# Performance work log

Hardware: AMD Instinct MI355X
Metric: run time of the kernel (lower is better)

## Reference

```python
import math
import jax, jax.numpy as jnp
import numpy as np

N_HEAD = 8
EPS = 1e-4

def _ln(x, g, b):
    m = jnp.mean(x, axis=-1, keepdims=True)
    v = jnp.mean((x - m) ** 2, axis=-1, keepdims=True)
    return (x - m) * jax.lax.rsqrt(v + EPS) * g + b

def _rel_bias(T, rel_w):
    # rel_pos_mat[i,j] = j - i, shifted to [0, 2T-2]; one-hot @ W == table lookup
    pos = jnp.arange(T)
    idx = pos[None, :] - pos[:, None] + (T - 1)        # [T,T]
    return rel_w[idx].transpose(2, 0, 1)               # [n_head,T,T]

def _attn(x, qw, qb, kw, kb, vw, vb, pw, pb, rel_pos):
    B, T, C = x.shape
    hd = C // N_HEAD
    q = (x @ qw + qb).reshape(B, T, N_HEAD, hd)
    k = (x @ kw + kb).reshape(B, T, N_HEAD, hd)
    v = (x @ vw + vb).reshape(B, T, N_HEAD, hd)
    att = jnp.einsum('bqhd,bkhd->bhqk', q, k) * (1.0 / math.sqrt(hd))
    att = att + rel_pos[None]
    att = jax.nn.softmax(att, axis=-1)
    y = jnp.einsum('bhqk,bkhd->bqhd', att, v).reshape(B, T, C)
    return y @ pw + pb

def setup_inputs() -> dict:
    key = jax.random.key(0)
    C, H, W, B = 512, 64, 64, 8
    ks = iter(jax.random.split(key, 40))
    d = {}
    d['x'] = jax.random.normal(next(ks), (B, H * W, C), jnp.float32)
    def w(shape):
        return jax.random.normal(next(ks), shape, jnp.float32) * 0.02
    for p in ('row', 'col'):
        for nm in ('q', 'k', 'v', 'p'):
            d[f'{p}_{nm}w'] = w((C, C))
            d[f'{p}_{nm}b'] = jnp.zeros((C,), jnp.float32)
    for nm in ('rln1', 'cln1', 'ln2'):
        d[f'{nm}_g'] = jnp.ones((C,), jnp.float32)
        d[f'{nm}_b'] = jnp.zeros((C,), jnp.float32)
    d['ff_w1'] = w((C, 4 * C)); d['ff_b1'] = jnp.zeros((4 * C,), jnp.float32)
    d['ff_w2'] = w((4 * C, C)); d['ff_b2'] = jnp.zeros((C,), jnp.float32)
    d['row_rel_w'] = w((2 * H - 1, N_HEAD))
    d['col_rel_w'] = w((2 * W - 1, N_HEAD))
    return d

def reference(x,
              row_qw, row_qb, row_kw, row_kb, row_vw, row_vb, row_pw, row_pb,
              col_qw, col_qb, col_kw, col_kb, col_vw, col_vb, col_pw, col_pb,
              rln1_g, rln1_b, cln1_g, cln1_b, ln2_g, ln2_b,
              ff_w1, ff_b1, ff_w2, ff_b2, row_rel_w, col_rel_w):
    b, n, c = x.shape
    h = w = int(math.isqrt(n))
    # row attention: over h within each column -> batch b*w
    xr = x.reshape(b, h, w, c).transpose(0, 2, 1, 3).reshape(b * w, h, c)
    x_row = _attn(_ln(xr, rln1_g, rln1_b),
                  row_qw, row_qb, row_kw, row_kb, row_vw, row_vb, row_pw, row_pb,
                  _rel_bias(h, row_rel_w))
    x_row = x_row.reshape(b, w, h, c).transpose(0, 2, 1, 3).reshape(b, h * w, c)
    # col attention: over w within each row -> batch b*h
    xc = xr.reshape(b, w, h, c).transpose(0, 2, 1, 3).reshape(b * h, w, c)
    x_col = _attn(_ln(xc, cln1_g, cln1_b),
                  col_qw, col_qb, col_kw, col_kb, col_vw, col_vb, col_pw, col_pb,
                  _rel_bias(w, col_rel_w))
    x_col = x_col.reshape(b, h * w, c)
    out = x + x_row + x_col
    hdd = _ln(out, ln2_g, ln2_b) @ ff_w1 + ff_b1
    hdd = jax.nn.gelu(hdd, approximate=False)
    out = out + (hdd @ ff_w2 + ff_b2)
    return out
```

## Files before the change

### kernel.cpp

```cpp
#include <hip/hip_runtime.h>

typedef unsigned short u16;
typedef unsigned int   u32;
typedef float  f32x4  __attribute__((ext_vector_type(4)));
typedef u32    u32x4  __attribute__((ext_vector_type(4)));
typedef __bf16 bf16x8 __attribute__((ext_vector_type(8)));

#define DEV __device__ __forceinline__

DEV float b2f(u16 u){ return __uint_as_float(((u32)u) << 16); }
DEV u16 f2b(float f){
  u32 u = __float_as_uint(f);
  u32 r = 0x7FFFu + ((u >> 16) & 1u);
  return (u16)((u + r) >> 16);
}
DEV u32 pack2(float a, float b){ return (u32)f2b(a) | ((u32)f2b(b) << 16); }
DEV uint4 pack8(const float* o){
  uint4 r;
  r.x = pack2(o[0], o[1]); r.y = pack2(o[2], o[3]);
  r.z = pack2(o[4], o[5]); r.w = pack2(o[6], o[7]);
  return r;
}

DEV f32x4 mfma16(u32x4 a, u32x4 b, f32x4 c){
  return __builtin_amdgcn_mfma_f32_16x16x32_bf16(
      __builtin_bit_cast(bf16x8, a), __builtin_bit_cast(bf16x8, b), c, 0, 0, 0);
}

DEV void gload16(const u16* g, u16* l){
  __builtin_amdgcn_global_load_lds((const __attribute__((address_space(1))) void*)(g),
                                   (__attribute__((address_space(3))) void*)(l), 16, 0, 0);
}

__global__ __launch_bounds__(256) void tranb3(
    const float* __restrict__ sA, const float* __restrict__ sB,
    const float* __restrict__ sC,
    u16* __restrict__ dA, u16* __restrict__ dB, u16* __restrict__ dC){
  __shared__ float tile[32][33];
  const float* src = (blockIdx.z == 0) ? sA : (blockIdx.z == 1) ? sB : sC;
  u16* dst = (blockIdx.z == 0) ? dA : (blockIdx.z == 1) ? dB : dC;
  const int bx = blockIdx.x * 32, by = blockIdx.y * 32;
  const int tx = threadIdx.x, ty = threadIdx.y;
#pragma unroll
  for (int i = 0; i < 4; ++i)
    tile[ty + i * 8][tx] = src[(size_t)(by + ty + i * 8) * 512 + bx + tx];
  __syncthreads();
#pragma unroll
  for (int i = 0; i < 4; ++i)
    dst[(size_t)(bx + ty + i * 8) * 512 + by + tx] = f2b(tile[tx][ty + i * 8]);
}

__global__ __launch_bounds__(256) void tranbP(const float* __restrict__ src,
                                              u16* __restrict__ dst, int off){
  __shared__ float tile[32][33];
  const int bx = blockIdx.x * 32, by = blockIdx.y * 32;
  const int tx = threadIdx.x, ty = threadIdx.y;
#pragma unroll
  for (int i = 0; i < 4; ++i)
    tile[ty + i * 8][tx] = src[(size_t)(by + ty + i * 8) * 512 + bx + tx];
  __syncthreads();
#pragma unroll
  for (int i = 0; i < 4; ++i)
    dst[(size_t)(bx + ty + i * 8) * 1024 + off + by + tx] = f2b(tile[tx][ty + i * 8]);
}

__global__ __launch_bounds__(256) void tranb(const float* __restrict__ src, u16* __restrict__ dst,
                                             int R, int C){
  __shared__ float tile[32][33];
  const int bx = blockIdx.x * 32, by = blockIdx.y * 32;
  const int tx = threadIdx.x, ty = threadIdx.y;
#pragma unroll
  for (int i = 0; i < 4; ++i)
    tile[ty + i * 8][tx] = src[(size_t)(by + ty + i * 8) * C + bx + tx];
  __syncthreads();
#pragma unroll
  for (int i = 0; i < 4; ++i)
    dst[(size_t)(bx + ty + i * 8) * R + by + tx] = f2b(tile[tx][ty + i * 8]);
}

template<int TWO>
__global__ __launch_bounds__(256) void ln_k(const float* __restrict__ x,
    const float* __restrict__ g1, const float* __restrict__ b1,
    const float* __restrict__ g2, const float* __restrict__ b2,
    u16* __restrict__ y1, u16* __restrict__ y2){
  const int tid = threadIdx.x, lane = tid & 63, wv = tid >> 6;
  const size_t row  = (size_t)blockIdx.x * 4 + wv;
  const size_t boff = row * 512 + lane * 8;
  float f[8];
  {
    const f32x4* p = (const f32x4*)(x + boff);
    const f32x4 a = p[0], b = p[1];
#pragma unroll
    for (int j = 0; j < 4; ++j){ f[j] = a[j]; f[4 + j] = b[j]; }
  }
  float s1 = 0.f, s2 = 0.f;
#pragma unroll
  for (int j = 0; j < 8; ++j){ s1 += f[j]; s2 += f[j] * f[j]; }
#pragma unroll
  for (int off = 32; off > 0; off >>= 1){
    s1 += __shfl_xor(s1, off);
    s2 += __shfl_xor(s2, off);
  }
  const float m   = s1 * (1.0f / 512.0f);
  const float var = s2 * (1.0f / 512.0f) - m * m;
  const float inv = rsqrtf(var + 1e-4f);
  const int cb = lane * 8;
  float o[8];
#pragma unroll
  for (int j = 0; j < 8; ++j) o[j] = (f[j] - m) * inv * g1[cb + j] + b1[cb + j];
  *(uint4*)(y1 + boff) = pack8(o);
  if (TWO){
#pragma unroll
    for (int j = 0; j < 8; ++j) o[j] = (f[j] - m) * inv * g2[cb + j] + b2[cb + j];
    *(uint4*)(y2 + boff) = pack8(o);
  }
}

template<int EPI, bool FUSE3>
__global__ __launch_bounds__(512, 2) void gemm128(const u16* __restrict__ A,
    const u16* __restrict__ A2nd, int nkA,
    const u16* __restrict__ Bt,
    const float* __restrict__ b0p, const float* __restrict__ b1p,
    const float* __restrict__ b2p,
    const float* __restrict__ res,
    void* __restrict__ out0, void* __restrict__ out1, void* __restrict__ out2,
    int Nd, int K, int lda){
  __shared__ __align__(16) u16 smem[32768];
  const int tid  = threadIdx.x;
  const int lane = tid & 63;
  const int lr = lane & 15, lg = lane >> 4;
  const int wave = tid >> 6;
  const int wm = (wave >> 2) * 64, wn = (wave & 3) * 32;
  const u32 fd  = blockIdx.y * gridDim.x + blockIdx.x;
  const u32 cpx = (gridDim.x * gridDim.y) >> 3;
  const u32 T   = (fd & 7) * cpx + (fd >> 3);
  const int m0 = (T / gridDim.x) * 128, n0 = (T % gridDim.x) * 128;
  const int nk = K >> 6;

  f32x4 acc[4][2] = {};

  auto stage = [&](int buf, int kt){
    const u16* Ap; int kb;
    if (kt < nkA){ Ap = A;    kb = kt * 64; }
    else         { Ap = A2nd; kb = (kt - nkA) * 64; }
    const int kbB = kt * 64;
    const int ao = buf * 8192, bo = 16384 + buf * 8192;
#pragma unroll
    for (int i = 0; i < 2; ++i){
      const int c = i * 512 + tid;
      const int r = c >> 3, gc = (c & 7) ^ (r & 7);
      gload16(Ap + (size_t)(m0 + r) * lda + kb + gc * 8, smem + ao + c * 8);
    }
#pragma unroll
    for (int i = 0; i < 2; ++i){
      const int c = i * 512 + tid;
      const int r = c >> 3, gc = (c & 7) ^ (r & 7);
      gload16(Bt + (size_t)(n0 + r) * K + kbB + gc * 8, smem + bo + c * 8);
    }
  };

  stage(0, 0);
  int cur = 0;
  for (int kt = 0; kt < nk; ++kt){
    if (kt + 1 < nk){
      stage(cur ^ 1, kt + 1);
      asm volatile("s_waitcnt vmcnt(4)" ::: "memory");
    } else {
      asm volatile("s_waitcnt vmcnt(0)" ::: "memory");
    }
    __builtin_amdgcn_s_barrier();
    __builtin_amdgcn_sched_barrier(0);
    const int ao = cur * 8192, bo = 16384 + cur * 8192;
#pragma unroll
    for (int kk = 0; kk < 2; ++kk){
      u32x4 af[4], bf[2];
#pragma unroll
      for (int t = 0; t < 4; ++t){
        const int js = (kk * 4 + lg) ^ (lr & 7);
        af[t] = *(const u32x4*)&smem[ao + (wm + t * 16 + lr) * 64 + js * 8];
      }
#pragma unroll
      for (int t = 0; t < 2; ++t){
        const int js = (kk * 4 + lg) ^ (lr & 7);
        bf[t] = *(const u32x4*)&smem[bo + (wn + t * 16 + lr) * 64 + js * 8];
      }
      __builtin_amdgcn_s_setprio(1);
#pragma unroll
      for (int mt = 0; mt < 4; ++mt)
#pragma unroll
        for (int nt = 0; nt < 2; ++nt)
          acc[mt][nt] = mfma16(af[mt], bf[nt], acc[mt][nt]);
      __builtin_amdgcn_s_setprio(0);
    }
    asm volatile("" ::: "memory");
    __builtin_amdgcn_sched_barrier(0);
    __builtin_amdgcn_s_barrier();
    cur ^= 1;
  }

  if (EPI == 2){
    float* Cf = (float*)smem;
#pragma unroll
    for (int mt = 0; mt < 4; ++mt)
#pragma unroll
      for (int nt = 0; nt < 2; ++nt){
        const int col = wn + nt * 16 + lr;
        float bv = b0p[n0 + col];
        if (b1p) bv += b1p[n0 + col];
#pragma unroll
        for (int r = 0; r < 4; ++r)
          Cf[(wm + mt * 16 + lg * 4 + r) * 128 + col] = acc[mt][nt][r] + bv;
      }
    __syncthreads();
    float* o = (float*)out0;
#pragma unroll
    for (int p = 0; p < 8; ++p){
      const int rr = p * 16 + (tid >> 5);
      const int cc = (tid & 31) * 4;
      f32x4 c = *(f32x4*)&Cf[rr * 128 + cc];
      const size_t gi = (size_t)(m0 + rr) * Nd + n0 + cc;
      c += *(const f32x4*)(res + gi);
      *(f32x4*)(o + gi) = c;
    }
  } else {
    u16* Cl = smem;
#pragma unroll
    for (int mt = 0; mt < 4; ++mt)
#pragma unroll
      for (int nt = 0; nt < 2; ++nt){
        const int col = n0 + wn + nt * 16 + lr;
        float bv;
        if (FUSE3){
          if (col >= 1024)      bv = b2p[col - 1024];
          else if (col >= 512)  bv = b1p[col - 512];
          else                  bv = b0p[col];
        } else bv = b0p[col];
#pragma unroll
        for (int r = 0; r < 4; ++r){
          float v2 = acc[mt][nt][r] + bv;
          if (EPI == 1) v2 = 0.5f * v2 * (1.0f + erff(v2 * 0.70710678118654752f));
          Cl[(wm + mt * 16 + lg * 4 + r) * 136 + wn + nt * 16 + lr] = f2b(v2);
        }
      }
    __syncthreads();
    u16* o = (u16*)out0;
    int ncol = n0;
    if (FUSE3){
      const int grp = n0 >> 9;
      o = (u16*)(grp == 0 ? out0 : grp == 1 ? out1 : out2);
      ncol = n0 & 511;
    }
#pragma unroll
    for (int p = 0; p < 4; ++p){
      const int rr = p * 32 + (tid >> 4);
      const int cc = (tid & 15) * 8;
      *(uint4*)(o + (size_t)(m0 + rr) * (FUSE3 ? 512 : Nd) + ncol + cc) =
          *(uint4*)&Cl[rr * 136 + cc];
    }
  }
}

__global__ __launch_bounds__(256, 2) void attn64(u16* __restrict__ q,
    const u16* __restrict__ k, const u16* __restrict__ v,
    const float* __restrict__ relw,
    int sscale, int tstr){
  __shared__ __align__(16) u16 Qs[64 * 80];
  __shared__ __align__(16) u16 Ks[64 * 80];
  __shared__ __align__(16) u16 Vt[64 * 80];
  __shared__ __align__(16) u16 Ps[64 * 80];
  __shared__ float Ss[64 * 68];
  __shared__ float tb[128];

  const int s = blockIdx.x, head = blockIdx.y;
  const int tid = threadIdx.x;
  const int lane = tid & 63, wv = tid >> 6;
  const int lr = lane & 15, lg = lane >> 4;
  const int base = (s >> 6) * 4096 + (s & 63) * sscale;

  if (tid < 127) tb[tid] = relw[tid * 8 + head];

#pragma unroll
  for (int rep = 0; rep < 2; ++rep){
    const int e = rep * 2048 + tid * 8;
    const int t = e >> 6, c = e & 63;
    const size_t goff = (size_t)(base + t * tstr) * 512 + head * 64 + c;
    *(uint4*)&Qs[t * 80 + c] = *(const uint4*)(q + goff);
    *(uint4*)&Ks[t * 80 + c] = *(const uint4*)(k + goff);
    const uint4 vvv = *(const uint4*)(v + goff);
    u32 w;
    w = vvv.x; Vt[(c + 0) * 80 + t] = (u16)w; Vt[(c + 1) * 80 + t] = (u16)(w >> 16);
    w = vvv.y; Vt[(c + 2) * 80 + t] = (u16)w; Vt[(c + 3) * 80 + t] = (u16)(w >> 16);
    w = vvv.z; Vt[(c + 4) * 80 + t] = (u16)w; Vt[(c + 5) * 80 + t] = (u16)(w >> 16);
    w = vvv.w; Vt[(c + 6) * 80 + t] = (u16)w; Vt[(c + 7) * 80 + t] = (u16)(w >> 16);
  }
  __syncthreads();

  const int i0 = wv * 16;
  u32x4 af[2];
#pragma unroll
  for (int kk = 0; kk < 2; ++kk)
    af[kk] = *(const u32x4*)&Qs[(i0 + lr) * 80 + kk * 32 + lg * 8];
#pragma unroll
  for (int jt = 0; jt < 4; ++jt){
    f32x4 acc = {};
#pragma unroll
    for (int kk = 0; kk < 2; ++kk){
      const u32x4 bf = *(const u32x4*)&Ks[(jt * 16 + lr) * 80 + kk * 32 + lg * 8];
      acc = mfma16(af[kk], bf, acc);
    }
#pragma unroll
    for (int r = 0; r < 4; ++r){
      const int i = i0 + lg * 4 + r;
      const int j = jt * 16 + lr;
      Ss[i * 68 + j] = acc[r] * 0.125f + tb[j - i + 63];
    }
  }
  __syncthreads();

  {
    const int rr = tid >> 2, cp = tid & 3;
    float ev[16];
    float mx = -3.0e38f;
#pragma unroll
    for (int u = 0; u < 16; ++u){ ev[u] = Ss[rr * 68 + cp * 16 + u]; mx = fmaxf(mx, ev[u]); }
    mx = fmaxf(mx, __shfl_xor(mx, 1, 4));
    mx = fmaxf(mx, __shfl_xor(mx, 2, 4));
    float sum = 0.f;
#pragma unroll
    for (int u = 0; u < 16; ++u){ ev[u] = expf(ev[u] - mx); sum += ev[u]; }
    sum += __shfl_xor(sum, 1, 4);
    sum += __shfl_xor(sum, 2, 4);
    const float inv = 1.0f / sum;
#pragma unroll
    for (int u = 0; u < 16; ++u) Ps[rr * 80 + cp * 16 + u] = f2b(ev[u] * inv);
  }
  __syncthreads();

  u32x4 pa[2];
#pragma unroll
  for (int kk = 0; kk < 2; ++kk)
    pa[kk] = *(const u32x4*)&Ps[(i0 + lr) * 80 + kk * 32 + lg * 8];
#pragma unroll
  for (int dt = 0; dt < 4; ++dt){
    f32x4 acc = {};
#pragma unroll
    for (int kk = 0; kk < 2; ++kk){
      const u32x4 bf = *(const u32x4*)&Vt[(dt * 16 + lr) * 80 + kk * 32 + lg * 8];
      acc = mfma16(pa[kk], bf, acc);
    }
#pragma unroll
    for (int r = 0; r < 4; ++r)
      Qs[(i0 + lg * 4 + r) * 80 + dt * 16 + lr] = f2b(acc[r]);
  }
  __syncthreads();

#pragma unroll
  for (int p = 0; p < 2; ++p){
    const int rr = p * 32 + (tid >> 3);
    const int cc = (tid & 7) * 8;
    *(uint4*)(q + (size_t)(base + rr * tstr) * 512 + head * 64 + cc) =
        *(uint4*)&Qs[rr * 80 + cc];
  }
}

extern "C" void kernel_launch(void* const* d_in, const int* in_sizes, int n_in,
                              void* d_out, int out_size, void* d_ws, size_t ws_size,
                              hipStream_t stream){
  const float* x      = (const float*)d_in[0];
  const float* row_qw = (const float*)d_in[1];  const float* row_qb = (const float*)d_in[2];
  const float* row_kw = (const float*)d_in[3];  const float* row_kb = (const float*)d_in[4];
  const float* row_vw = (const float*)d_in[5];  const float* row_vb = (const float*)d_in[6];
  const float* row_pw = (const float*)d_in[7];  const float* row_pb = (const float*)d_in[8];
  const float* col_qw = (const float*)d_in[9];  const float* col_qb = (const float*)d_in[10];
  const float* col_kw = (const float*)d_in[11]; const float* col_kb = (const float*)d_in[12];
  const float* col_vw = (const float*)d_in[13]; const float* col_vb = (const float*)d_in[14];
  const float* col_pw = (const float*)d_in[15]; const float* col_pb = (const float*)d_in[16];
  const float* rg  = (const float*)d_in[17]; const float* rb  = (const float*)d_in[18];
  const float* cg  = (const float*)d_in[19]; const float* cb  = (const float*)d_in[20];
  const float* l2g = (const float*)d_in[21]; const float* l2b = (const float*)d_in[22];
  const float* ffw1 = (const float*)d_in[23]; const float* ffb1 = (const float*)d_in[24];
  const float* ffw2 = (const float*)d_in[25]; const float* ffb2 = (const float*)d_in[26];
  const float* rrel = (const float*)d_in[27]; const float* crel = (const float*)d_in[28];
  float* outp = (float*)d_out;
  u16* outp16 = (u16*)d_out;

  const size_t ACT = (size_t)32768 * 512;
  const size_t W55 = (size_t)512 * 512;
  const size_t NEED = (4 * ACT + 8 * W55) * 2;
  if (ws_size < NEED) return;

  u16* A0 = (u16*)d_ws;
  u16* A1 = A0 + ACT;
  u16* A2 = A1 + ACT;
  u16* A3 = A2 + ACT;
  u16* D0 = outp16;
  u16* D1 = outp16 + ACT;
  u16* wtb = A3 + ACT;
  u16* wt_q = wtb;  u16* wt_k = wtb + W55;  u16* wt_v = wtb + 2 * W55;
  u16* wt_p = wtb + 3 * W55;
  u16* f1t  = wtb;
  u16* f2t  = wtb + 4 * W55;

  const dim3 tpb(32, 8);
  const dim3 gQKV(12, 256);
  const dim3 gProj(4, 256);
  const dim3 gAttn(512, 8);

  ln_k<1><<<8192, 256, 0, stream>>>(x, rg, rb, cg, cb, A0, D0);

  tranb3<<<dim3(16, 16, 3), tpb, 0, stream>>>(row_qw, row_kw, row_vw, wt_q, wt_k, wt_v);
  tranbP<<<dim3(16, 16), tpb, 0, stream>>>(row_pw, wt_p, 0);
  gemm128<0, true><<<gQKV, 512, 0, stream>>>(A0, A0, 99, wt_q, row_qb, row_kb, row_vb,
                                             nullptr, A1, A2, A3, 512, 512, 512);
  attn64<<<gAttn, 256, 0, stream>>>(A1, A2, A3, rrel, 1, 64);

  tranb3<<<dim3(16, 16, 3), tpb, 0, stream>>>(col_qw, col_kw, col_vw, wt_q, wt_k, wt_v);
  tranbP<<<dim3(16, 16), tpb, 0, stream>>>(col_pw, wt_p, 512);
  gemm128<0, true><<<gQKV, 512, 0, stream>>>(D0, D0, 99, wt_q, col_qb, col_kb, col_vb,
                                             nullptr, A2, A3, D1, 512, 512, 512);
  attn64<<<gAttn, 256, 0, stream>>>(A2, A3, D1, crel, 64, 1);

  gemm128<2, false><<<gProj, 512, 0, stream>>>(A1, A2, 8, wt_p, row_pb, col_pb,
                                               nullptr, x, outp, nullptr, nullptr,
                                               512, 1024, 512);

  ln_k<0><<<8192, 256, 0, stream>>>(outp, l2g, l2b, nullptr, nullptr, A0, nullptr);
  tranb<<<dim3(64, 16), tpb, 0, stream>>>(ffw1, f1t, 512, 2048);
  tranb<<<dim3(16, 64), tpb, 0, stream>>>(ffw2, f2t, 2048, 512);
  for (int c = 0; c < 2; ++c){
    const size_t ro = (size_t)c * 16384;
    gemm128<1, false><<<dim3(16, 128), 512, 0, stream>>>(A0 + ro * 512, A0, 99, f1t,
        ffb1, nullptr, nullptr, nullptr, A1, nullptr, nullptr, 2048, 512, 512);
    gemm128<2, false><<<dim3(4, 128), 512, 0, stream>>>(A1, A1, 99, f2t,
        ffb2, nullptr, nullptr, outp + ro * 512, outp + ro * 512, nullptr, nullptr,
        512, 2048, 2048);
  }
}
```

Before: 473.1 us.

## Add 256x256-tile GEMM kernel for QKV, projection and FFN1 GEMMs

Introduces a gemm256 kernel with 256x256 output tiles (each of 8 waves computes 128x64) and uses it for the fused QKV, output projection and FFN1 GEMMs. The older gemm128 is kept, simplified, for FFN2 only. Larger tiles raise arithmetic intensity and halve global reloads of A and B per output element. In exchange they use 128KB of LDS and many more accumulator registers, which can limit occupancy, and the grids shrink (e.g. 768 blocks for QKV), which reduces wave-level parallelism.

```diff
diff --git a/kernel.cpp b/kernel.cpp
--- a/kernel.cpp
+++ b/kernel.cpp
@@ -117,13 +117,160 @@
 }
 
 template<int EPI, bool FUSE3>
-__global__ __launch_bounds__(512, 2) void gemm128(const u16* __restrict__ A,
+__global__ __launch_bounds__(512, 2) void gemm256(const u16* __restrict__ A,
     const u16* __restrict__ A2nd, int nkA,
     const u16* __restrict__ Bt,
     const float* __restrict__ b0p, const float* __restrict__ b1p,
     const float* __restrict__ b2p,
     const float* __restrict__ res,
     void* __restrict__ out0, void* __restrict__ out1, void* __restrict__ out2,
+    int Nd, int K, int lda){
+  __shared__ __align__(16) u16 smem[65536];
+  const int tid  = threadIdx.x;
+  const int lane = tid & 63;
+  const int lr = lane & 15, lg = lane >> 4;
+  const int wave = tid >> 6;
+  const int wm = (wave >> 2) * 128, wn = (wave & 3) * 64;
+  const u32 fd  = blockIdx.y * gridDim.x + blockIdx.x;
+  const u32 cpx = (gridDim.x * gridDim.y) >> 3;
+  const u32 T   = (fd & 7) * cpx + (fd >> 3);
+  const int m0 = (T / gridDim.x) * 256, n0 = (T % gridDim.x) * 256;
+  const int nk = K >> 6;
+
+  f32x4 acc[8][4] = {};
+
+  auto stage = [&](int buf, int kt){
+    const u16* Ap; int kb;
+    if (kt < nkA){ Ap = A;    kb = kt * 64; }
+    else         { Ap = A2nd; kb = (kt - nkA) * 64; }
+    const int kbB = kt * 64;
+    const int ao = buf * 16384, bo = 32768 + buf * 16384;
+#pragma unroll
+    for (int i = 0; i < 4; ++i){
+      const int c = i * 512 + tid;
+      const int r = c >> 3, gc = (c & 7) ^ (r & 7);
+      gload16(Ap + (size_t)(m0 + r) * lda + kb + gc * 8, smem + ao + c * 8);
+    }
+#pragma unroll
+    for (int i = 0; i < 4; ++i){
+      const int c = i * 512 + tid;
+      const int r = c >> 3, gc = (c & 7) ^ (r & 7);
+      gload16(Bt + (size_t)(n0 + r) * K + kbB + gc * 8, smem + bo + c * 8);
+    }
+  };
+
+  stage(0, 0);
+  int cur = 0;
+  for (int kt = 0; kt < nk; ++kt){
+    if (kt + 1 < nk){
+      stage(cur ^ 1, kt + 1);
+      asm volatile("s_waitcnt vmcnt(8)" ::: "memory");
+    } else {
+      asm volatile("s_waitcnt vmcnt(0)" ::: "memory");
+    }
+    __builtin_amdgcn_s_barrier();
+    __builtin_amdgcn_sched_barrier(0);
+    const int ao = cur * 16384, bo = 32768 + cur * 16384;
+#pragma unroll
+    for (int kk = 0; kk < 2; ++kk){
+      const int js = (kk * 4 + lg) ^ (lr & 7);
+      u32x4 bf[4], af[4];
+#pragma unroll
+      for (int nt = 0; nt < 4; ++nt)
+        bf[nt] = *(const u32x4*)&smem[bo + (wn + nt * 16 + lr) * 64 + js * 8];
+#pragma unroll
+      for (int mh = 0; mh < 2; ++mh){
+#pragma unroll
+        for (int mt = 0; mt < 4; ++mt)
+          af[mt] = *(const u32x4*)&smem[ao + (wm + mh * 64 + mt * 16 + lr) * 64 + js * 8];
+        __builtin_amdgcn_s_setprio(1);
+#pragma unroll
+        for (int mt = 0; mt < 4; ++mt)
+#pragma unroll
+          for (int nt = 0; nt < 4; ++nt)
+            acc[mh * 4 + mt][nt] = mfma16(af[mt], bf[nt], acc[mh * 4 + mt][nt]);
+        __builtin_amdgcn_s_setprio(0);
+      }
+    }
+    asm volatile("" ::: "memory");
+    __builtin_amdgcn_sched_barrier(0);
+    __builtin_amdgcn_s_barrier();
+    cur ^= 1;
+  }
+
+  if (EPI == 2){
+    float* Cf = (float*)smem;
+    float* o = (float*)out0;
+#pragma unroll
+    for (int h = 0; h < 2; ++h){
+      if ((wave >> 2) == h){
+#pragma unroll
+        for (int m = 0; m < 8; ++m)
+#pragma unroll
+          for (int nt = 0; nt < 4; ++nt){
+            const int col = wn + nt * 16 + lr;
+            float bv = b0p[n0 + col];
+            if (b1p) bv += b1p[n0 + col];
+#pragma unroll
+            for (int r = 0; r < 4; ++r)
+              Cf[(m * 16 + lg * 4 + r) * 256 + col] = acc[m][nt][r] + bv;
+          }
+      }
+      __syncthreads();
+#pragma unroll
+      for (int p = 0; p < 16; ++p){
+        const int rr = p * 8 + (tid >> 6);
+        const int cc = (tid & 63) * 4;
+        f32x4 c = *(f32x4*)&Cf[rr * 256 + cc];
+        const size_t gi = (size_t)(m0 + h * 128 + rr) * Nd + n0 + cc;
+        c += *(const f32x4*)(res + gi);
+        *(f32x4*)(o + gi) = c;
+      }
+      __syncthreads();
+    }
+  } else {
+    u16* Cl = smem;
+#pragma unroll
+    for (int m = 0; m < 8; ++m)
+#pragma unroll
+      for (int nt = 0; nt < 4; ++nt){
+        const int col = n0 + wn + nt * 16 + lr;
+        float bv;
+        if (FUSE3){
+          if (col >= 1024)      bv = b2p[col - 1024];
+          else if (col >= 512)  bv = b1p[col - 512];
+          else                  bv = b0p[col];
+        } else bv = b0p[col];
+#pragma unroll
+        for (int r = 0; r < 4; ++r){
+          float v2 = acc[m][nt][r] + bv;
+          if (EPI == 1) v2 = 0.5f * v2 * (1.0f + erff(v2 * 0.70710678118654752f));
+          Cl[(wm + m * 16 + lg * 4 + r) * 256 + wn + nt * 16 + lr] = f2b(v2);
+        }
+      }
+    __syncthreads();
+    u16* o = (u16*)out0;
+    int ncol = n0;
+    if (FUSE3){
+      const int grp = n0 >> 9;
+      o = (u16*)(grp == 0 ? out0 : grp == 1 ? out1 : out2);
+      ncol = n0 & 511;
+    }
+#pragma unroll
+    for (int p = 0; p < 16; ++p){
+      const int rr = p * 16 + (tid >> 5);
+      const int cc = (tid & 31) * 8;
+      *(uint4*)(o + (size_t)(m0 + rr) * (FUSE3 ? 512 : Nd) + ncol + cc) =
+          *(uint4*)&Cl[rr * 256 + cc];
+    }
+  }
+}
+
+template<int EPI>
+__global__ __launch_bounds__(512, 2) void gemm128(const u16* __restrict__ A,
+    const u16* __restrict__ Bt,
+    const float* __restrict__ b0p,
+    const float* __restrict__ res, void* __restrict__ outv,
     int Nd, int K, int lda){
   __shared__ __align__(16) u16 smem[32768];
   const int tid  = threadIdx.x;
@@ -140,22 +287,19 @@
   f32x4 acc[4][2] = {};
 
   auto stage = [&](int buf, int kt){
-    const u16* Ap; int kb;
-    if (kt < nkA){ Ap = A;    kb = kt * 64; }
-    else         { Ap = A2nd; kb = (kt - nkA) * 64; }
-    const int kbB = kt * 64;
+    const int kb = kt * 64;
     const int ao = buf * 8192, bo = 16384 + buf * 8192;
 #pragma unroll
     for (int i = 0; i < 2; ++i){
       const int c = i * 512 + tid;
       const int r = c >> 3, gc = (c & 7) ^ (r & 7);
-      gload16(Ap + (size_t)(m0 + r) * lda + kb + gc * 8, smem + ao + c * 8);
+      gload16(A + (size_t)(m0 + r) * lda + kb + gc * 8, smem + ao + c * 8);
     }
 #pragma unroll
     for (int i = 0; i < 2; ++i){
       const int c = i * 512 + tid;
       const int r = c >> 3, gc = (c & 7) ^ (r & 7);
-      gload16(Bt + (size_t)(n0 + r) * K + kbB + gc * 8, smem + bo + c * 8);
+      gload16(Bt + (size_t)(n0 + r) * K + kb + gc * 8, smem + bo + c * 8);
     }
   };
 
@@ -205,14 +349,13 @@
 #pragma unroll
       for (int nt = 0; nt < 2; ++nt){
         const int col = wn + nt * 16 + lr;
-        float bv = b0p[n0 + col];
-        if (b1p) bv += b1p[n0 + col];
+        const float bv = b0p[n0 + col];
 #pragma unroll
         for (int r = 0; r < 4; ++r)
           Cf[(wm + mt * 16 + lg * 4 + r) * 128 + col] = acc[mt][nt][r] + bv;
       }
     __syncthreads();
-    float* o = (float*)out0;
+    float* o = (float*)outv;
 #pragma unroll
     for (int p = 0; p < 8; ++p){
       const int rr = p * 16 + (tid >> 5);
@@ -229,12 +372,7 @@
 #pragma unroll
       for (int nt = 0; nt < 2; ++nt){
         const int col = n0 + wn + nt * 16 + lr;
-        float bv;
-        if (FUSE3){
-          if (col >= 1024)      bv = b2p[col - 1024];
-          else if (col >= 512)  bv = b1p[col - 512];
-          else                  bv = b0p[col];
-        } else bv = b0p[col];
+        const float bv = b0p[col];
 #pragma unroll
         for (int r = 0; r < 4; ++r){
           float v2 = acc[mt][nt][r] + bv;
@@ -243,19 +381,12 @@
         }
       }
     __syncthreads();
-    u16* o = (u16*)out0;
-    int ncol = n0;
-    if (FUSE3){
-      const int grp = n0 >> 9;
-      o = (u16*)(grp == 0 ? out0 : grp == 1 ? out1 : out2);
-      ncol = n0 & 511;
-    }
+    u16* o = (u16*)outv;
 #pragma unroll
     for (int p = 0; p < 4; ++p){
       const int rr = p * 32 + (tid >> 4);
       const int cc = (tid & 15) * 8;
-      *(uint4*)(o + (size_t)(m0 + rr) * (FUSE3 ? 512 : Nd) + ncol + cc) =
-          *(uint4*)&Cl[rr * 136 + cc];
+      *(uint4*)(o + (size_t)(m0 + rr) * Nd + n0 + cc) = *(uint4*)&Cl[rr * 136 + cc];
     }
   }
 }
@@ -402,25 +533,25 @@
   u16* f2t  = wtb + 4 * W55;
 
   const dim3 tpb(32, 8);
-  const dim3 gQKV(12, 256);
-  const dim3 gProj(4, 256);
+  const dim3 gQKV(6, 128);
+  const dim3 gProj(2, 128);
   const dim3 gAttn(512, 8);
 
   ln_k<1><<<8192, 256, 0, stream>>>(x, rg, rb, cg, cb, A0, D0);
 
   tranb3<<<dim3(16, 16, 3), tpb, 0, stream>>>(row_qw, row_kw, row_vw, wt_q, wt_k, wt_v);
   tranbP<<<dim3(16, 16), tpb, 0, stream>>>(row_pw, wt_p, 0);
-  gemm128<0, true><<<gQKV, 512, 0, stream>>>(A0, A0, 99, wt_q, row_qb, row_kb, row_vb,
+  gemm256<0, true><<<gQKV, 512, 0, stream>>>(A0, A0, 99, wt_q, row_qb, row_kb, row_vb,
                                              nullptr, A1, A2, A3, 512, 512, 512);
   attn64<<<gAttn, 256, 0, stream>>>(A1, A2, A3, rrel, 1, 64);
 
   tranb3<<<dim3(16, 16, 3), tpb, 0, stream>>>(col_qw, col_kw, col_vw, wt_q, wt_k, wt_v);
   tranbP<<<dim3(16, 16), tpb, 0, stream>>>(col_pw, wt_p, 512);
-  gemm128<0, true><<<gQKV, 512, 0, stream>>>(D0, D0, 99, wt_q, col_qb, col_kb, col_vb,
+  gemm256<0, true><<<gQKV, 512, 0, stream>>>(D0, D0, 99, wt_q, col_qb, col_kb, col_vb,
                                              nullptr, A2, A3, D1, 512, 512, 512);
   attn64<<<gAttn, 256, 0, stream>>>(A2, A3, D1, crel, 64, 1);
 
-  gemm128<2, false><<<gProj, 512, 0, stream>>>(A1, A2, 8, wt_p, row_pb, col_pb,
+  gemm256<2, false><<<gProj, 512, 0, stream>>>(A1, A2, 8, wt_p, row_pb, col_pb,
                                                nullptr, x, outp, nullptr, nullptr,
                                                512, 1024, 512);
 
@@ -429,10 +560,9 @@
   tranb<<<dim3(16, 64), tpb, 0, stream>>>(ffw2, f2t, 2048, 512);
   for (int c = 0; c < 2; ++c){
     const size_t ro = (size_t)c * 16384;
-    gemm128<1, false><<<dim3(16, 128), 512, 0, stream>>>(A0 + ro * 512, A0, 99, f1t,
+    gemm256<1, false><<<dim3(8, 64), 512, 0, stream>>>(A0 + ro * 512, A0, 99, f1t,
         ffb1, nullptr, nullptr, nullptr, A1, nullptr, nullptr, 2048, 512, 512);
-    gemm128<2, false><<<dim3(4, 128), 512, 0, stream>>>(A1, A1, 99, f2t,
-        ffb2, nullptr, nullptr, outp + ro * 512, outp + ro * 512, nullptr, nullptr,
-        512, 2048, 2048);
-  }
-}
+    gemm128<2><<<dim3(4, 128), 512, 0, stream>>>(A1, f2t,
+        ffb2, outp + ro * 512, outp + ro * 512, 512, 2048, 2048);
+  }
+}
```

New measurement: 608.8 us. +28.7%, slower.

## Widen GEMM tiles to 128x256 with K=32 stages and split FFN by hidden halves

Applied to the files above, without the earlier changes.

The GEMM kernel now uses 128x256 output tiles, with each wave computing a 64x64 sub-tile and K-steps of 32, and a new XOR swizzle for the 32-wide rows. The aim is to raise MFMA work per LDS load. The FFN is no longer chunked over rows. It is split over the hidden dimension into two 1024-wide halves, with the second FF2 half accumulating into the output, so each launch covers all 32768 rows. The wider tiles raise register pressure per thread, and the launch-bounds hint of 4 blocks may force spills. The FP32 epilogue now runs in two serialized halves.

```diff
diff --git a/kernel.cpp b/kernel.cpp
--- a/kernel.cpp
+++ b/kernel.cpp
@@ -117,9 +117,9 @@
 }
 
 template<int EPI, bool FUSE3>
-__global__ __launch_bounds__(512, 2) void gemm128(const u16* __restrict__ A,
+__global__ __launch_bounds__(512, 4) void gemmW(const u16* __restrict__ A,
     const u16* __restrict__ A2nd, int nkA,
-    const u16* __restrict__ Bt,
+    const u16* __restrict__ Bt, int ldb,
     const float* __restrict__ b0p, const float* __restrict__ b1p,
     const float* __restrict__ b2p,
     const float* __restrict__ res,
@@ -130,32 +130,30 @@
   const int lane = tid & 63;
   const int lr = lane & 15, lg = lane >> 4;
   const int wave = tid >> 6;
-  const int wm = (wave >> 2) * 64, wn = (wave & 3) * 32;
+  const int wm = (wave >> 2) * 64, wn = (wave & 3) * 64;
   const u32 fd  = blockIdx.y * gridDim.x + blockIdx.x;
   const u32 cpx = (gridDim.x * gridDim.y) >> 3;
   const u32 T   = (fd & 7) * cpx + (fd >> 3);
-  const int m0 = (T / gridDim.x) * 128, n0 = (T % gridDim.x) * 128;
-  const int nk = K >> 6;
-
-  f32x4 acc[4][2] = {};
+  const int m0 = (T / gridDim.x) * 128, n0 = (T % gridDim.x) * 256;
+  const int nk = K >> 5;
+
+  f32x4 acc[4][4] = {};
 
   auto stage = [&](int buf, int kt){
     const u16* Ap; int kb;
-    if (kt < nkA){ Ap = A;    kb = kt * 64; }
-    else         { Ap = A2nd; kb = (kt - nkA) * 64; }
-    const int kbB = kt * 64;
-    const int ao = buf * 8192, bo = 16384 + buf * 8192;
+    if (kt < nkA){ Ap = A;    kb = kt * 32; }
+    else         { Ap = A2nd; kb = (kt - nkA) * 32; }
+    const int kbB = kt * 32;
+    const int ao = buf * 12288, bo = ao + 4096;
+    {
+      const int r = tid >> 2, gc = (tid & 3) ^ ((r >> 1) & 3);
+      gload16(Ap + (size_t)(m0 + r) * lda + kb + gc * 8, smem + ao + tid * 8);
+    }
 #pragma unroll
     for (int i = 0; i < 2; ++i){
       const int c = i * 512 + tid;
-      const int r = c >> 3, gc = (c & 7) ^ (r & 7);
-      gload16(Ap + (size_t)(m0 + r) * lda + kb + gc * 8, smem + ao + c * 8);
-    }
-#pragma unroll
-    for (int i = 0; i < 2; ++i){
-      const int c = i * 512 + tid;
-      const int r = c >> 3, gc = (c & 7) ^ (r & 7);
-      gload16(Bt + (size_t)(n0 + r) * K + kbB + gc * 8, smem + bo + c * 8);
+      const int r = c >> 2, gc = (c & 3) ^ ((r >> 1) & 3);
+      gload16(Bt + (size_t)(n0 + r) * ldb + kbB + gc * 8, smem + bo + c * 8);
     }
   };
 
@@ -164,34 +162,33 @@
   for (int kt = 0; kt < nk; ++kt){
     if (kt + 1 < nk){
       stage(cur ^ 1, kt + 1);
-      asm volatile("s_waitcnt vmcnt(4)" ::: "memory");
+      asm volatile("s_waitcnt vmcnt(3)" ::: "memory");
     } else {
       asm volatile("s_waitcnt vmcnt(0)" ::: "memory");
     }
     __builtin_amdgcn_s_barrier();
     __builtin_amdgcn_sched_barrier(0);
-    const int ao = cur * 8192, bo = 16384 + cur * 8192;
-#pragma unroll
-    for (int kk = 0; kk < 2; ++kk){
-      u32x4 af[4], bf[2];
-#pragma unroll
-      for (int t = 0; t < 4; ++t){
-        const int js = (kk * 4 + lg) ^ (lr & 7);
-        af[t] = *(const u32x4*)&smem[ao + (wm + t * 16 + lr) * 64 + js * 8];
-      }
-#pragma unroll
-      for (int t = 0; t < 2; ++t){
-        const int js = (kk * 4 + lg) ^ (lr & 7);
-        bf[t] = *(const u32x4*)&smem[bo + (wn + t * 16 + lr) * 64 + js * 8];
-      }
-      __builtin_amdgcn_s_setprio(1);
-#pragma unroll
-      for (int mt = 0; mt < 4; ++mt)
-#pragma unroll
-        for (int nt = 0; nt < 2; ++nt)
-          acc[mt][nt] = mfma16(af[mt], bf[nt], acc[mt][nt]);
-      __builtin_amdgcn_s_setprio(0);
-    }
+    const int ao = cur * 12288, bo = ao + 4096;
+    u32x4 af[4], bf[4];
+#pragma unroll
+    for (int mt = 0; mt < 4; ++mt){
+      const int row = wm + mt * 16 + lr;
+      const int js = lg ^ ((row >> 1) & 3);
+      af[mt] = *(const u32x4*)&smem[ao + row * 32 + js * 8];
+    }
+#pragma unroll
+    for (int nt = 0; nt < 4; ++nt){
+      const int row = wn + nt * 16 + lr;
+      const int js = lg ^ ((row >> 1) & 3);
+      bf[nt] = *(const u32x4*)&smem[bo + row * 32 + js * 8];
+    }
+    __builtin_amdgcn_s_setprio(1);
+#pragma unroll
+    for (int mt = 0; mt < 4; ++mt)
+#pragma unroll
+      for (int nt = 0; nt < 4; ++nt)
+        acc[mt][nt] = mfma16(af[mt], bf[nt], acc[mt][nt]);
+    __builtin_amdgcn_s_setprio(0);
     asm volatile("" ::: "memory");
     __builtin_amdgcn_sched_barrier(0);
     __builtin_amdgcn_s_barrier();
@@ -200,34 +197,40 @@
 
   if (EPI == 2){
     float* Cf = (float*)smem;
-#pragma unroll
-    for (int mt = 0; mt < 4; ++mt)
-#pragma unroll
-      for (int nt = 0; nt < 2; ++nt){
-        const int col = wn + nt * 16 + lr;
-        float bv = b0p[n0 + col];
-        if (b1p) bv += b1p[n0 + col];
-#pragma unroll
-        for (int r = 0; r < 4; ++r)
-          Cf[(wm + mt * 16 + lg * 4 + r) * 128 + col] = acc[mt][nt][r] + bv;
+    float* o = (float*)out0;
+#pragma unroll
+    for (int h = 0; h < 2; ++h){
+      if ((wave >> 2) == h){
+#pragma unroll
+        for (int mt = 0; mt < 4; ++mt)
+#pragma unroll
+          for (int nt = 0; nt < 4; ++nt){
+            const int col = wn + nt * 16 + lr;
+            float bv = b0p ? b0p[n0 + col] : 0.0f;
+            if (b1p) bv += b1p[n0 + col];
+#pragma unroll
+            for (int r = 0; r < 4; ++r)
+              Cf[(mt * 16 + lg * 4 + r) * 256 + col] = acc[mt][nt][r] + bv;
+          }
       }
-    __syncthreads();
-    float* o = (float*)out0;
-#pragma unroll
-    for (int p = 0; p < 8; ++p){
-      const int rr = p * 16 + (tid >> 5);
-      const int cc = (tid & 31) * 4;
-      f32x4 c = *(f32x4*)&Cf[rr * 128 + cc];
-      const size_t gi = (size_t)(m0 + rr) * Nd + n0 + cc;
-      c += *(const f32x4*)(res + gi);
-      *(f32x4*)(o + gi) = c;
+      __syncthreads();
+#pragma unroll
+      for (int p = 0; p < 8; ++p){
+        const int rr = p * 8 + (tid >> 6);
+        const int cc = (tid & 63) * 4;
+        f32x4 c = *(f32x4*)&Cf[rr * 256 + cc];
+        const size_t gi = (size_t)(m0 + h * 64 + rr) * Nd + n0 + cc;
+        c += *(const f32x4*)(res + gi);
+        *(f32x4*)(o + gi) = c;
+      }
+      __syncthreads();
     }
   } else {
     u16* Cl = smem;
 #pragma unroll
     for (int mt = 0; mt < 4; ++mt)
 #pragma unroll
-      for (int nt = 0; nt < 2; ++nt){
+      for (int nt = 0; nt < 4; ++nt){
         const int col = n0 + wn + nt * 16 + lr;
         float bv;
         if (FUSE3){
@@ -239,7 +242,7 @@
         for (int r = 0; r < 4; ++r){
           float v2 = acc[mt][nt][r] + bv;
           if (EPI == 1) v2 = 0.5f * v2 * (1.0f + erff(v2 * 0.70710678118654752f));
-          Cl[(wm + mt * 16 + lg * 4 + r) * 136 + wn + nt * 16 + lr] = f2b(v2);
+          Cl[(wm + mt * 16 + lg * 4 + r) * 256 + wn + nt * 16 + lr] = f2b(v2);
         }
       }
     __syncthreads();
@@ -251,11 +254,11 @@
       ncol = n0 & 511;
     }
 #pragma unroll
-    for (int p = 0; p < 4; ++p){
-      const int rr = p * 32 + (tid >> 4);
-      const int cc = (tid & 15) * 8;
+    for (int p = 0; p < 8; ++p){
+      const int rr = p * 16 + (tid >> 5);
+      const int cc = (tid & 31) * 8;
       *(uint4*)(o + (size_t)(m0 + rr) * (FUSE3 ? 512 : Nd) + ncol + cc) =
-          *(uint4*)&Cl[rr * 136 + cc];
+          *(uint4*)&Cl[rr * 256 + cc];
     }
   }
 }
@@ -400,39 +403,41 @@
   u16* wt_p = wtb + 3 * W55;
   u16* f1t  = wtb;
   u16* f2t  = wtb + 4 * W55;
+  u16* hid  = A1;
 
   const dim3 tpb(32, 8);
-  const dim3 gQKV(12, 256);
-  const dim3 gProj(4, 256);
+  const dim3 gQKV(6, 256);
+  const dim3 gProj(2, 256);
+  const dim3 gFF1(4, 256);
+  const dim3 gFF2(2, 256);
   const dim3 gAttn(512, 8);
 
   ln_k<1><<<8192, 256, 0, stream>>>(x, rg, rb, cg, cb, A0, D0);
 
   tranb3<<<dim3(16, 16, 3), tpb, 0, stream>>>(row_qw, row_kw, row_vw, wt_q, wt_k, wt_v);
   tranbP<<<dim3(16, 16), tpb, 0, stream>>>(row_pw, wt_p, 0);
-  gemm128<0, true><<<gQKV, 512, 0, stream>>>(A0, A0, 99, wt_q, row_qb, row_kb, row_vb,
-                                             nullptr, A1, A2, A3, 512, 512, 512);
+  gemmW<0, true><<<gQKV, 512, 0, stream>>>(A0, A0, 999, wt_q, 512,
+      row_qb, row_kb, row_vb, nullptr, A1, A2, A3, 512, 512, 512);
   attn64<<<gAttn, 256, 0, stream>>>(A1, A2, A3, rrel, 1, 64);
 
   tranb3<<<dim3(16, 16, 3), tpb, 0, stream>>>(col_qw, col_kw, col_vw, wt_q, wt_k, wt_v);
   tranbP<<<dim3(16, 16), tpb, 0, stream>>>(col_pw, wt_p, 512);
-  gemm128<0, true><<<gQKV, 512, 0, stream>>>(D0, D0, 99, wt_q, col_qb, col_kb, col_vb,
-                                             nullptr, A2, A3, D1, 512, 512, 512);
+  gemmW<0, true><<<gQKV, 512, 0, stream>>>(D0, D0, 999, wt_q, 512,
+      col_qb, col_kb, col_vb, nullptr, A2, A3, D1, 512, 512, 512);
   attn64<<<gAttn, 256, 0, stream>>>(A2, A3, D1, crel, 64, 1);
 
-  gemm128<2, false><<<gProj, 512, 0, stream>>>(A1, A2, 8, wt_p, row_pb, col_pb,
-                                               nullptr, x, outp, nullptr, nullptr,
-                                               512, 1024, 512);
+  gemmW<2, false><<<gProj, 512, 0, stream>>>(A1, A2, 16, wt_p, 1024,
+      row_pb, col_pb, nullptr, x, outp, nullptr, nullptr, 512, 1024, 512);
 
   ln_k<0><<<8192, 256, 0, stream>>>(outp, l2g, l2b, nullptr, nullptr, A0, nullptr);
   tranb<<<dim3(64, 16), tpb, 0, stream>>>(ffw1, f1t, 512, 2048);
   tranb<<<dim3(16, 64), tpb, 0, stream>>>(ffw2, f2t, 2048, 512);
-  for (int c = 0; c < 2; ++c){
-    const size_t ro = (size_t)c * 16384;
-    gemm128<1, false><<<dim3(16, 128), 512, 0, stream>>>(A0 + ro * 512, A0, 99, f1t,
-        ffb1, nullptr, nullptr, nullptr, A1, nullptr, nullptr, 2048, 512, 512);
-    gemm128<2, false><<<dim3(4, 128), 512, 0, stream>>>(A1, A1, 99, f2t,
-        ffb2, nullptr, nullptr, outp + ro * 512, outp + ro * 512, nullptr, nullptr,
-        512, 2048, 2048);
-  }
-}
+  gemmW<1, false><<<gFF1, 512, 0, stream>>>(A0, A0, 999, f1t, 512,
+      ffb1, nullptr, nullptr, nullptr, hid, nullptr, nullptr, 1024, 512, 512);
+  gemmW<2, false><<<gFF2, 512, 0, stream>>>(hid, hid, 999, f2t, 2048,
+      ffb2, nullptr, nullptr, outp, outp, nullptr, nullptr, 512, 1024, 1024);
+  gemmW<1, false><<<gFF1, 512, 0, stream>>>(A0, A0, 999, f1t + (size_t)1024 * 512, 512,
+      ffb1 + 1024, nullptr, nullptr, nullptr, hid, nullptr, nullptr, 1024, 512, 512);
+  gemmW<2, false><<<gFF2, 512, 0, stream>>>(hid, hid, 999, f2t + 1024, 2048,
+      nullptr, nullptr, nullptr, outp, outp, nullptr, nullptr, 512, 1024, 1024);
+}
```

Result: slower. 499.1 us (+5.5%).
